# Performance work log

Measured on AMD Instinct MI355X. Metric: run time of the kernel, lower is better.

The kernel has to match this reference:

```python
import jax, jax.numpy as jnp
import numpy as np

N = 500_000
E = 8_000_000
DIM = 3
CG_ITERS = 20
CG_TOL = 1e-4


def setup_inputs() -> dict:
    key = jax.random.key(0)
    k0, k1, k2, k3, k4, k5 = jax.random.split(key, 6)
    u_hat = jax.random.normal(k0, (N, DIM), dtype=jnp.float32)
    edge_index = jax.random.randint(k1, (2, E), 0, N, dtype=jnp.int32)
    face_normals = jax.random.normal(k2, (E, DIM), dtype=jnp.float32)
    face_areas = jax.random.uniform(k3, (E,), dtype=jnp.float32)
    face_dists = jax.random.uniform(k4, (E,), dtype=jnp.float32)
    cell_volumes = jax.random.uniform(k5, (N,), dtype=jnp.float32)
    return {
        "u_hat": u_hat,
        "edge_index": edge_index,
        "face_normals": face_normals,
        "face_areas": face_areas,
        "face_dists": face_dists,
        "cell_volumes": cell_volumes,
    }


def _segsum(vals, idx, n):
    return jax.ops.segment_sum(vals, idx, num_segments=n)


def reference(u_hat, edge_index, face_normals, face_areas, face_dists, cell_volumes):
    src, dst = edge_index[0], edge_index[1]
    n = u_hat.shape[0]

    # --- compute_divergence: D_i = (1/V_i) sum flux over faces into i ---
    u_face = 0.5 * (u_hat[src] + u_hat[dst])                 # (E, dim)
    flux = jnp.sum(u_face * face_normals, axis=-1) * face_areas  # (E,)
    div = _segsum(flux, dst, n) / jnp.clip(cell_volumes, 1e-12)

    # --- build_laplacian_rhs ---
    w = face_areas / jnp.clip(face_dists, 1e-8)              # (E,)
    diag = _segsum(w, dst, n)                                # (N,)
    off = -w
    b = div

    # --- cg_solve with Jacobi preconditioner ---
    m_inv = 1.0 / jnp.clip(diag, 1e-8)

    def matvec(phi):
        return diag * phi + _segsum(off * phi[src], dst, n)

    phi0 = jnp.zeros_like(b)
    r0 = b - matvec(phi0)
    z0 = m_inv * r0
    p0 = z0
    rz0 = jnp.sum(r0 * z0)

    def step(state, _):
        phi, r, z, p, rz, done = state
        # torch checks ||r|| < tol and breaks before the update
        active = jnp.logical_and(~done, jnp.linalg.norm(r) >= CG_TOL)
        ap = matvec(p)
        alpha = rz / (jnp.sum(p * ap) + 1e-12)
        phi_n = phi + alpha * p
        r_n = r - alpha * ap
        z_n = m_inv * r_n
        rz_n = jnp.sum(r_n * z_n)
        beta = rz_n / (rz + 1e-12)
        p_n = z_n + beta * p
        sel = lambda a, b_: jnp.where(active, a, b_)
        new_state = (sel(phi_n, phi), sel(r_n, r), sel(z_n, z),
                     sel(p_n, p), jnp.where(active, rz_n, rz), ~active)
        return new_state, None

    (phi, _, _, _, _, _), _ = jax.lax.scan(
        step, (phi0, r0, z0, p0, rz0, jnp.array(False)), None, length=CG_ITERS)

    # --- apply_pressure_correction ---
    grad_term = (w * phi[src])[:, None] * face_normals       # (E, dim)
    grad_phi = _segsum(grad_term, dst, n) / jnp.clip(cell_volumes, 1e-12)[:, None]
    u_corrected = u_hat - grad_phi
    return u_corrected, phi
```

## Files before the change

kernel.cpp:

```cpp
#include <hip/hip_runtime.h>


#define TPB 256
#define KB 2048
#define CG_ITERS 20
#define TOL2 1e-8f

struct Sum3 { float a, b, c; };

__device__ inline Sum3 block_sum3_bcast(const float* __restrict__ A,
                                        const float* __restrict__ B,
                                        const float* __restrict__ C, int n) {
  float va = 0.f, vb = 0.f, vc = 0.f;
  for (int k = threadIdx.x; k < n; k += TPB) { va += A[k]; vb += B[k]; vc += C[k]; }
#pragma unroll
  for (int o = 32; o; o >>= 1) {
    va += __shfl_down(va, o, 64);
    vb += __shfl_down(vb, o, 64);
    vc += __shfl_down(vc, o, 64);
  }
  __shared__ float sa[TPB / 64], sb[TPB / 64], sc[TPB / 64], bc[3];
  int lane = threadIdx.x & 63, wid = threadIdx.x >> 6;
  if (lane == 0) { sa[wid] = va; sb[wid] = vb; sc[wid] = vc; }
  __syncthreads();
  if (threadIdx.x == 0) {
    float ta = 0.f, tb = 0.f, tc = 0.f;
#pragma unroll
    for (int k = 0; k < TPB / 64; k++) { ta += sa[k]; tb += sb[k]; tc += sc[k]; }
    bc[0] = ta; bc[1] = tb; bc[2] = tc;
  }
  __syncthreads();
  Sum3 r{bc[0], bc[1], bc[2]};
  __syncthreads();
  return r;
}

__device__ inline void block_reduce1_store(float v1, float* d1) {
#pragma unroll
  for (int o = 32; o; o >>= 1) v1 += __shfl_down(v1, o, 64);
  __shared__ float s1[TPB / 64];
  int lane = threadIdx.x & 63, wid = threadIdx.x >> 6;
  if (lane == 0) s1[wid] = v1;
  __syncthreads();
  if (threadIdx.x == 0) {
    float t1 = 0.f;
#pragma unroll
    for (int k = 0; k < TPB / 64; k++) t1 += s1[k];
    *d1 = t1;
  }
}

__device__ inline void block_reduce2_store(float v1, float v2, float* d1, float* d2) {
#pragma unroll
  for (int o = 32; o; o >>= 1) {
    v1 += __shfl_down(v1, o, 64);
    v2 += __shfl_down(v2, o, 64);
  }
  __shared__ float s1[TPB / 64], s2[TPB / 64];
  int lane = threadIdx.x & 63, wid = threadIdx.x >> 6;
  if (lane == 0) { s1[wid] = v1; s2[wid] = v2; }
  __syncthreads();
  if (threadIdx.x == 0) {
    float t1 = 0.f, t2 = 0.f;
#pragma unroll
    for (int k = 0; k < TPB / 64; k++) { t1 += s1[k]; t2 += s2[k]; }
    *d1 = t1;
    *d2 = t2;
  }
}

__global__ __launch_bounds__(TPB) void hist(
    const int* __restrict__ ei, unsigned* __restrict__ cnt,
    unsigned* __restrict__ rank, int E) {
  int e = blockIdx.x * TPB + threadIdx.x;
  if (e >= E) return;
  rank[e] = atomicAdd(&cnt[ei[E + e]], 1u);
}

__global__ __launch_bounds__(TPB) void scan_blocks(
    const unsigned* __restrict__ cnt, unsigned* __restrict__ offs,
    unsigned* __restrict__ btot, int n) {
  __shared__ unsigned sd[TPB];
  int t = threadIdx.x;
  int base = blockIdx.x * 1024 + t * 4;
  unsigned v0 = 0, v1 = 0, v2 = 0, v3 = 0;
  if (base + 0 < n) v0 = cnt[base + 0];
  if (base + 1 < n) v1 = cnt[base + 1];
  if (base + 2 < n) v2 = cnt[base + 2];
  if (base + 3 < n) v3 = cnt[base + 3];
  unsigned local = v0 + v1 + v2 + v3;
  sd[t] = local;
  __syncthreads();
  for (int o = 1; o < TPB; o <<= 1) {
    unsigned x = (t >= o) ? sd[t - o] : 0u;
    __syncthreads();
    sd[t] += x;
    __syncthreads();
  }
  unsigned excl = sd[t] - local;
  if (base + 0 < n) offs[base + 0] = excl; excl += v0;
  if (base + 1 < n) offs[base + 1] = excl; excl += v1;
  if (base + 2 < n) offs[base + 2] = excl; excl += v2;
  if (base + 3 < n) offs[base + 3] = excl;
  if (t == TPB - 1) btot[blockIdx.x] = sd[TPB - 1];
}

__global__ __launch_bounds__(512) void scan_totals(unsigned* __restrict__ btot, int nb) {
  __shared__ unsigned sd[512];
  int t = threadIdx.x;
  unsigned v = (t < nb) ? btot[t] : 0u;
  sd[t] = v;
  __syncthreads();
  for (int o = 1; o < 512; o <<= 1) {
    unsigned x = (t >= o) ? sd[t - o] : 0u;
    __syncthreads();
    sd[t] += x;
    __syncthreads();
  }
  if (t < nb) btot[t] = sd[t] - v;
}

__global__ __launch_bounds__(TPB) void scan_add(
    unsigned* __restrict__ offs, const unsigned* __restrict__ btot,
    int n, unsigned total) {
  int i = blockIdx.x * TPB + threadIdx.x;
  if (i < n) offs[i] += btot[i >> 10];
  if (i == 0) offs[n] = total;
}

__global__ __launch_bounds__(TPB) void scatter_edges(
    const int* __restrict__ ei, const float* __restrict__ u_hat,
    const float* __restrict__ fn, const float* __restrict__ fa,
    const float* __restrict__ fd, const unsigned* __restrict__ rank,
    const unsigned* __restrict__ offs, int2* __restrict__ csr_sw,
    int2* __restrict__ csr_ef, int E) {
  int e = blockIdx.x * TPB + threadIdx.x;
  if (e >= E) return;
  int s = ei[e], d = ei[E + e];
  float area = fa[e];
  float w = area / fmaxf(fd[e], 1e-8f);
  float ux = 0.5f * (u_hat[3 * s]     + u_hat[3 * d]);
  float uy = 0.5f * (u_hat[3 * s + 1] + u_hat[3 * d + 1]);
  float uz = 0.5f * (u_hat[3 * s + 2] + u_hat[3 * d + 2]);
  float flux = (ux * fn[3 * e] + uy * fn[3 * e + 1] + uz * fn[3 * e + 2]) * area;
  unsigned pos = offs[d] + rank[e];
  csr_sw[pos] = make_int2(s, __float_as_int(w));
  csr_ef[pos] = make_int2(e, __float_as_int(flux));
}

__global__ __launch_bounds__(TPB) void node_setup(
    const int2* __restrict__ csr_sw, const int2* __restrict__ csr_ef,
    const unsigned* __restrict__ offs, const float* __restrict__ cv,
    float* __restrict__ diag, float* __restrict__ r, float* __restrict__ p,
    float* __restrict__ phi, float* __restrict__ minv,
    float* __restrict__ rz_part, float* __restrict__ rr_part, int N) {
  const int gpb = TPB / 8;
  const int stride = KB * gpb;
  int g0 = blockIdx.x * gpb + (threadIdx.x >> 3);
  int l = threadIdx.x & 7;
  float rzacc = 0.f, rracc = 0.f;
  for (int g = g0; g < N; g += stride) {
    unsigned a = offs[g], bnd = offs[g + 1];
    float wsum = 0.f, fsum = 0.f;
    for (unsigned j = a + l; j < bnd; j += 8) {
      wsum += __int_as_float(csr_sw[j].y);
      fsum += __int_as_float(csr_ef[j].y);
    }
#pragma unroll
    for (int o = 4; o; o >>= 1) {
      wsum += __shfl_down(wsum, o, 8);
      fsum += __shfl_down(fsum, o, 8);
    }
    if (l == 0) {
      float vol = fmaxf(cv[g], 1e-12f);
      float b = fsum / vol;
      float mi = 1.0f / fmaxf(wsum, 1e-8f);
      diag[g] = wsum;
      minv[g] = mi;
      r[g] = b;
      phi[g] = 0.f;
      float pi = mi * b;
      p[g] = pi;
      rzacc += b * pi;
      rracc += b * b;
    }
  }
  block_reduce2_store(rzacc, rracc, &rz_part[blockIdx.x], &rr_part[blockIdx.x]);
}

__global__ __launch_bounds__(TPB) void matvec(
    const float* __restrict__ p, const float* __restrict__ diag,
    const unsigned* __restrict__ offs, const int2* __restrict__ csr_sw,
    float* __restrict__ ap, float* __restrict__ pap_part, int N) {
  const int gpb = TPB / 8;
  const int stride = KB * gpb;
  int g0 = blockIdx.x * gpb + (threadIdx.x >> 3);
  int l = threadIdx.x & 7;
  float acc = 0.f;
  for (int g = g0; g < N; g += stride) {
    unsigned a = offs[g], bnd = offs[g + 1];
    float sum = 0.f;
    for (unsigned j = a + l; j < bnd; j += 8) {
      int2 sw = csr_sw[j];
      sum += __int_as_float(sw.y) * p[sw.x];
    }
#pragma unroll
    for (int o = 4; o; o >>= 1) sum += __shfl_down(sum, o, 8);
    if (l == 0) {
      float pi = p[g];
      float api = diag[g] * pi - sum;
      ap[g] = api;
      acc += pi * api;
    }
  }
  block_reduce1_store(acc, &pap_part[blockIdx.x]);
}

__global__ __launch_bounds__(TPB) void cg_update(
    float* __restrict__ phi, float* __restrict__ r, const float* __restrict__ p,
    const float* __restrict__ ap, const float* __restrict__ minv,
    const float* __restrict__ pap_it, const float* __restrict__ rz_it,
    const float* __restrict__ rr_it, float* __restrict__ rz_next,
    float* __restrict__ rr_next, int N) {
  Sum3 s = block_sum3_bcast(pap_it, rz_it, rr_it, KB);
  bool act = (s.c >= TOL2);
  float alpha = s.b / (s.a + 1e-12f);
  float rzacc = 0.f, rracc = 0.f;
  for (int i = blockIdx.x * TPB + threadIdx.x; i < N; i += KB * TPB) {
    float ri = r[i];
    if (act) {
      phi[i] += alpha * p[i];
      ri -= alpha * ap[i];
      r[i] = ri;
    }
    float zi = minv[i] * ri;
    rzacc += ri * zi;
    rracc += ri * ri;
  }
  block_reduce2_store(rzacc, rracc, &rz_next[blockIdx.x], &rr_next[blockIdx.x]);
}

__global__ __launch_bounds__(TPB) void p_update(
    float* __restrict__ p, const float* __restrict__ r,
    const float* __restrict__ minv, const float* __restrict__ rz_next,
    const float* __restrict__ rz_it, const float* __restrict__ rr_it, int N) {
  Sum3 s = block_sum3_bcast(rz_next, rz_it, rr_it, KB);
  if (s.c < TOL2) return;
  float beta = s.a / (s.b + 1e-12f);
  for (int i = blockIdx.x * TPB + threadIdx.x; i < N; i += KB * TPB) {
    p[i] = minv[i] * r[i] + beta * p[i];
  }
}

__global__ __launch_bounds__(TPB) void finalize(
    const float* __restrict__ u_hat, const float* __restrict__ cv,
    const float* __restrict__ phi, const unsigned* __restrict__ offs,
    const int2* __restrict__ csr_sw, const int2* __restrict__ csr_ef,
    const float* __restrict__ fn, float* __restrict__ out, int N) {
  const int gpb = TPB / 8;
  const int stride = KB * gpb;
  int g0 = blockIdx.x * gpb + (threadIdx.x >> 3);
  int l = threadIdx.x & 7;
  for (int g = g0; g < N; g += stride) {
    unsigned a = offs[g], bnd = offs[g + 1];
    float gx = 0.f, gy = 0.f, gz = 0.f;
    for (unsigned j = a + l; j < bnd; j += 8) {
      int2 sw = csr_sw[j];
      float t = __int_as_float(sw.y) * phi[sw.x];
      int e = csr_ef[j].x;
      gx += t * fn[3 * e];
      gy += t * fn[3 * e + 1];
      gz += t * fn[3 * e + 2];
    }
#pragma unroll
    for (int o = 4; o; o >>= 1) {
      gx += __shfl_down(gx, o, 8);
      gy += __shfl_down(gy, o, 8);
      gz += __shfl_down(gz, o, 8);
    }
    if (l == 0) {
      float iv = 1.0f / fmaxf(cv[g], 1e-12f);
      out[3 * g]     = u_hat[3 * g]     - gx * iv;
      out[3 * g + 1] = u_hat[3 * g + 1] - gy * iv;
      out[3 * g + 2] = u_hat[3 * g + 2] - gz * iv;
      out[3 * N + g] = phi[g];
    }
  }
}

extern "C" void kernel_launch(void* const* d_in, const int* in_sizes, int n_in,
                              void* d_out, int out_size, void* d_ws, size_t ws_size,
                              hipStream_t stream) {
  const float* u_hat = (const float*)d_in[0];
  const int*   ei    = (const int*)d_in[1];
  const float* fn    = (const float*)d_in[2];
  const float* fa    = (const float*)d_in[3];
  const float* fd    = (const float*)d_in[4];
  const float* cv    = (const float*)d_in[5];
  float* out = (float*)d_out;

  const int N = in_sizes[0] / 3;
  const int E = in_sizes[1] / 2;

  char* base = (char*)d_ws;
  size_t off = 0;
  auto alloc = [&](size_t bytes) -> void* {
    void* ptr = base + off;
    off = (off + bytes + 255) & ~size_t(255);
    return ptr;
  };
  unsigned* cnt = (unsigned*)alloc((size_t)N * 4);
  size_t zero_bytes = off;
  unsigned* offs     = (unsigned*)alloc((size_t)(N + 1) * 4);
  unsigned* btot     = (unsigned*)alloc(512 * 4);
  unsigned* rank     = (unsigned*)alloc((size_t)E * 4);
  float*    diag     = (float*)alloc((size_t)N * 4);
  float*    minv     = (float*)alloc((size_t)N * 4);
  float*    phi      = (float*)alloc((size_t)N * 4);
  float*    rvec     = (float*)alloc((size_t)N * 4);
  float*    pvec     = (float*)alloc((size_t)N * 4);
  float*    ap       = (float*)alloc((size_t)N * 4);
  float*    rzrr     = (float*)alloc((size_t)(2 * (CG_ITERS + 1)) * KB * 4);
  float*    papp     = (float*)alloc((size_t)CG_ITERS * KB * 4);
  int2*     csr_sw   = (int2*)alloc((size_t)E * 8);
  int2*     csr_ef   = (int2*)alloc((size_t)E * 8);
  (void)ws_size; (void)n_in; (void)out_size;

  auto rz_part = [&](int it) { return rzrr + (size_t)(2 * it) * KB; };
  auto rr_part = [&](int it) { return rzrr + (size_t)(2 * it + 1) * KB; };
  auto pap_part = [&](int it) { return papp + (size_t)it * KB; };

  const int gridE = (E + TPB - 1) / TPB;
  const int gridN = (N + TPB - 1) / TPB;
  const int nbScan = (N + 1023) / 1024;

  hipMemsetAsync(base, 0, zero_bytes, stream);

  hist<<<gridE, TPB, 0, stream>>>(ei, cnt, rank, E);

  scan_blocks<<<nbScan, TPB, 0, stream>>>(cnt, offs, btot, N);
  scan_totals<<<1, 512, 0, stream>>>(btot, nbScan);
  scan_add<<<gridN, TPB, 0, stream>>>(offs, btot, N, (unsigned)E);

  scatter_edges<<<gridE, TPB, 0, stream>>>(ei, u_hat, fn, fa, fd, rank, offs,
                                           csr_sw, csr_ef, E);

  node_setup<<<KB, TPB, 0, stream>>>(csr_sw, csr_ef, offs, cv, diag,
                                     rvec, pvec, phi, minv,
                                     rz_part(0), rr_part(0), N);

  for (int it = 0; it < CG_ITERS; it++) {
    matvec<<<KB, TPB, 0, stream>>>(pvec, diag, offs, csr_sw, ap,
                                   pap_part(it), N);
    cg_update<<<KB, TPB, 0, stream>>>(phi, rvec, pvec, ap, minv,
                                      pap_part(it), rz_part(it), rr_part(it),
                                      rz_part(it + 1), rr_part(it + 1), N);
    if (it < CG_ITERS - 1) {
      p_update<<<KB, TPB, 0, stream>>>(pvec, rvec, minv,
                                       rz_part(it + 1), rz_part(it),
                                       rr_part(it), N);
    }
  }

  finalize<<<KB, TPB, 0, stream>>>(u_hat, cv, phi, offs, csr_sw, csr_ef,
                                   fn, out, N);
}
```

Before: 2.630 ms.

## Replace per-node CSR with 256-node bucketed edge layout and shared-memory accumulation

Edges are now grouped into buckets of 256 destination nodes with a two-pass, block-local counting sort. The old global-atomic histogram and per-edge rank array are gone. The source index and local destination are packed into one 64-bit word alongside the weight. The matvec, setup and finalize kernels process one bucket per block and accumulate into per-node shared-memory slots with LDS atomics, instead of 8-lane segmented reductions per node. This is meant to cut global atomic contention, remove divergence from variable row lengths, and shrink edge metadata traffic. The cost is LDS atomic contention and floating-point summation order that is no longer deterministic.

```diff
diff --git a/kernel.cpp b/kernel.cpp
--- a/kernel.cpp
+++ b/kernel.cpp
@@ -2,7 +2,10 @@
 
 
 #define TPB 256
+#define TPB_A 1024
 #define KB 2048
+#define NBLK 256
+#define MAXNB 2048
 #define CG_ITERS 20
 #define TOL2 1e-8f
 
@@ -69,12 +72,19 @@
   }
 }
 
-__global__ __launch_bounds__(TPB) void hist(
-    const int* __restrict__ ei, unsigned* __restrict__ cnt,
-    unsigned* __restrict__ rank, int E) {
-  int e = blockIdx.x * TPB + threadIdx.x;
-  if (e >= E) return;
-  rank[e] = atomicAdd(&cnt[ei[E + e]], 1u);
+__global__ __launch_bounds__(TPB_A) void bucket_hist(
+    const int* __restrict__ ei, unsigned* __restrict__ mat,
+    int E, int NB, int chunk) {
+  __shared__ unsigned cntL[MAXNB];
+  for (int i = threadIdx.x; i < NB; i += TPB_A) cntL[i] = 0;
+  __syncthreads();
+  int blk = blockIdx.x;
+  int e0 = blk * chunk, e1 = min(E, e0 + chunk);
+  for (int e = e0 + threadIdx.x; e < e1; e += TPB_A)
+    atomicAdd(&cntL[((unsigned)ei[E + e]) >> 8], 1u);
+  __syncthreads();
+  for (int b = threadIdx.x; b < NB; b += TPB_A)
+    mat[(size_t)b * NBLK + blk] = cntL[b];
 }
 
 __global__ __launch_bounds__(TPB) void scan_blocks(
@@ -128,92 +138,108 @@
   if (i == 0) offs[n] = total;
 }
 
-__global__ __launch_bounds__(TPB) void scatter_edges(
+__global__ __launch_bounds__(TPB_A) void bucket_place(
     const int* __restrict__ ei, const float* __restrict__ u_hat,
     const float* __restrict__ fn, const float* __restrict__ fa,
-    const float* __restrict__ fd, const unsigned* __restrict__ rank,
-    const unsigned* __restrict__ offs, int2* __restrict__ csr_sw,
-    int2* __restrict__ csr_ef, int E) {
-  int e = blockIdx.x * TPB + threadIdx.x;
-  if (e >= E) return;
-  int s = ei[e], d = ei[E + e];
-  float area = fa[e];
-  float w = area / fmaxf(fd[e], 1e-8f);
-  float ux = 0.5f * (u_hat[3 * s]     + u_hat[3 * d]);
-  float uy = 0.5f * (u_hat[3 * s + 1] + u_hat[3 * d + 1]);
-  float uz = 0.5f * (u_hat[3 * s + 2] + u_hat[3 * d + 2]);
-  float flux = (ux * fn[3 * e] + uy * fn[3 * e + 1] + uz * fn[3 * e + 2]) * area;
-  unsigned pos = offs[d] + rank[e];
-  csr_sw[pos] = make_int2(s, __float_as_int(w));
-  csr_ef[pos] = make_int2(e, __float_as_int(flux));
+    const float* __restrict__ fd, const unsigned* __restrict__ offs,
+    unsigned long long* __restrict__ A1, float* __restrict__ A2flux,
+    int* __restrict__ A3eid, int E, int NB, int chunk) {
+  __shared__ unsigned cntL[MAXNB];
+  __shared__ unsigned offL[MAXNB];
+  int blk = blockIdx.x;
+  for (int i = threadIdx.x; i < NB; i += TPB_A) {
+    cntL[i] = 0;
+    offL[i] = offs[(size_t)i * NBLK + blk];
+  }
+  __syncthreads();
+  int e0 = blk * chunk, e1 = min(E, e0 + chunk);
+  for (int e = e0 + threadIdx.x; e < e1; e += TPB_A) {
+    int s = ei[e], d = ei[E + e];
+    float area = fa[e];
+    float w = area / fmaxf(fd[e], 1e-8f);
+    float ux = 0.5f * (u_hat[3 * s]     + u_hat[3 * d]);
+    float uy = 0.5f * (u_hat[3 * s + 1] + u_hat[3 * d + 1]);
+    float uz = 0.5f * (u_hat[3 * s + 2] + u_hat[3 * d + 2]);
+    float flux = (ux * fn[3 * e] + uy * fn[3 * e + 1] + uz * fn[3 * e + 2]) * area;
+    unsigned b = ((unsigned)d) >> 8;
+    unsigned dl = ((unsigned)d) & 255u;
+    unsigned r = atomicAdd(&cntL[b], 1u);
+    unsigned pos = offL[b] + r;
+    unsigned hi = (dl << 19) | (unsigned)s;
+    A1[pos] = ((unsigned long long)hi << 32) | (unsigned long long)__float_as_uint(w);
+    A2flux[pos] = flux;
+    A3eid[pos] = e;
+  }
 }
 
 __global__ __launch_bounds__(TPB) void node_setup(
-    const int2* __restrict__ csr_sw, const int2* __restrict__ csr_ef,
+    const unsigned long long* __restrict__ A1, const float* __restrict__ A2flux,
     const unsigned* __restrict__ offs, const float* __restrict__ cv,
     float* __restrict__ diag, float* __restrict__ r, float* __restrict__ p,
     float* __restrict__ phi, float* __restrict__ minv,
-    float* __restrict__ rz_part, float* __restrict__ rr_part, int N) {
-  const int gpb = TPB / 8;
-  const int stride = KB * gpb;
-  int g0 = blockIdx.x * gpb + (threadIdx.x >> 3);
-  int l = threadIdx.x & 7;
-  float rzacc = 0.f, rracc = 0.f;
-  for (int g = g0; g < N; g += stride) {
-    unsigned a = offs[g], bnd = offs[g + 1];
-    float wsum = 0.f, fsum = 0.f;
-    for (unsigned j = a + l; j < bnd; j += 8) {
-      wsum += __int_as_float(csr_sw[j].y);
-      fsum += __int_as_float(csr_ef[j].y);
-    }
-#pragma unroll
-    for (int o = 4; o; o >>= 1) {
-      wsum += __shfl_down(wsum, o, 8);
-      fsum += __shfl_down(fsum, o, 8);
-    }
-    if (l == 0) {
-      float vol = fmaxf(cv[g], 1e-12f);
-      float b = fsum / vol;
+    float* __restrict__ rz_part, float* __restrict__ rr_part, int N, int NB) {
+  __shared__ float wacc[256], facc[256];
+  int b = blockIdx.x;
+  float rzv = 0.f, rrv = 0.f;
+  if (b < NB) {
+    wacc[threadIdx.x] = 0.f;
+    facc[threadIdx.x] = 0.f;
+    __syncthreads();
+    unsigned jb = offs[(size_t)b * NBLK], je = offs[(size_t)(b + 1) * NBLK];
+    for (unsigned j = jb + threadIdx.x; j < je; j += TPB) {
+      unsigned long long v = A1[j];
+      unsigned hi = (unsigned)(v >> 32);
+      float w = __uint_as_float((unsigned)v);
+      atomicAdd(&wacc[hi >> 19], w);
+      atomicAdd(&facc[hi >> 19], A2flux[j]);
+    }
+    __syncthreads();
+    int node = (b << 8) + threadIdx.x;
+    if (node < N) {
+      float wsum = wacc[threadIdx.x];
+      float vol = fmaxf(cv[node], 1e-12f);
+      float bval = facc[threadIdx.x] / vol;
       float mi = 1.0f / fmaxf(wsum, 1e-8f);
-      diag[g] = wsum;
-      minv[g] = mi;
-      r[g] = b;
-      phi[g] = 0.f;
-      float pi = mi * b;
-      p[g] = pi;
-      rzacc += b * pi;
-      rracc += b * b;
-    }
-  }
-  block_reduce2_store(rzacc, rracc, &rz_part[blockIdx.x], &rr_part[blockIdx.x]);
+      diag[node] = wsum;
+      minv[node] = mi;
+      r[node] = bval;
+      phi[node] = 0.f;
+      float pi = mi * bval;
+      p[node] = pi;
+      rzv = bval * pi;
+      rrv = bval * bval;
+    }
+  }
+  block_reduce2_store(rzv, rrv, &rz_part[blockIdx.x], &rr_part[blockIdx.x]);
 }
 
 __global__ __launch_bounds__(TPB) void matvec(
     const float* __restrict__ p, const float* __restrict__ diag,
-    const unsigned* __restrict__ offs, const int2* __restrict__ csr_sw,
-    float* __restrict__ ap, float* __restrict__ pap_part, int N) {
-  const int gpb = TPB / 8;
-  const int stride = KB * gpb;
-  int g0 = blockIdx.x * gpb + (threadIdx.x >> 3);
-  int l = threadIdx.x & 7;
-  float acc = 0.f;
-  for (int g = g0; g < N; g += stride) {
-    unsigned a = offs[g], bnd = offs[g + 1];
-    float sum = 0.f;
-    for (unsigned j = a + l; j < bnd; j += 8) {
-      int2 sw = csr_sw[j];
-      sum += __int_as_float(sw.y) * p[sw.x];
-    }
-#pragma unroll
-    for (int o = 4; o; o >>= 1) sum += __shfl_down(sum, o, 8);
-    if (l == 0) {
-      float pi = p[g];
-      float api = diag[g] * pi - sum;
-      ap[g] = api;
-      acc += pi * api;
-    }
-  }
-  block_reduce1_store(acc, &pap_part[blockIdx.x]);
+    const unsigned* __restrict__ offs, const unsigned long long* __restrict__ A1,
+    float* __restrict__ ap, float* __restrict__ pap_part, int N, int NB) {
+  __shared__ float acc[256];
+  int b = blockIdx.x;
+  float contrib = 0.f;
+  if (b < NB) {
+    acc[threadIdx.x] = 0.f;
+    __syncthreads();
+    unsigned jb = offs[(size_t)b * NBLK], je = offs[(size_t)(b + 1) * NBLK];
+    for (unsigned j = jb + threadIdx.x; j < je; j += TPB) {
+      unsigned long long v = A1[j];
+      unsigned hi = (unsigned)(v >> 32);
+      float w = __uint_as_float((unsigned)v);
+      atomicAdd(&acc[hi >> 19], w * p[hi & 0x7FFFFu]);
+    }
+    __syncthreads();
+    int node = (b << 8) + threadIdx.x;
+    if (node < N) {
+      float pi = p[node];
+      float api = diag[node] * pi - acc[threadIdx.x];
+      ap[node] = api;
+      contrib = pi * api;
+    }
+  }
+  block_reduce1_store(contrib, &pap_part[blockIdx.x]);
 }
 
 __global__ __launch_bounds__(TPB) void cg_update(
@@ -255,36 +281,35 @@
 __global__ __launch_bounds__(TPB) void finalize(
     const float* __restrict__ u_hat, const float* __restrict__ cv,
     const float* __restrict__ phi, const unsigned* __restrict__ offs,
-    const int2* __restrict__ csr_sw, const int2* __restrict__ csr_ef,
-    const float* __restrict__ fn, float* __restrict__ out, int N) {
-  const int gpb = TPB / 8;
-  const int stride = KB * gpb;
-  int g0 = blockIdx.x * gpb + (threadIdx.x >> 3);
-  int l = threadIdx.x & 7;
-  for (int g = g0; g < N; g += stride) {
-    unsigned a = offs[g], bnd = offs[g + 1];
-    float gx = 0.f, gy = 0.f, gz = 0.f;
-    for (unsigned j = a + l; j < bnd; j += 8) {
-      int2 sw = csr_sw[j];
-      float t = __int_as_float(sw.y) * phi[sw.x];
-      int e = csr_ef[j].x;
-      gx += t * fn[3 * e];
-      gy += t * fn[3 * e + 1];
-      gz += t * fn[3 * e + 2];
-    }
-#pragma unroll
-    for (int o = 4; o; o >>= 1) {
-      gx += __shfl_down(gx, o, 8);
-      gy += __shfl_down(gy, o, 8);
-      gz += __shfl_down(gz, o, 8);
-    }
-    if (l == 0) {
-      float iv = 1.0f / fmaxf(cv[g], 1e-12f);
-      out[3 * g]     = u_hat[3 * g]     - gx * iv;
-      out[3 * g + 1] = u_hat[3 * g + 1] - gy * iv;
-      out[3 * g + 2] = u_hat[3 * g + 2] - gz * iv;
-      out[3 * N + g] = phi[g];
-    }
+    const unsigned long long* __restrict__ A1, const int* __restrict__ A3eid,
+    const float* __restrict__ fn, float* __restrict__ out, int N, int NB) {
+  __shared__ float gxa[256], gya[256], gza[256];
+  int b = blockIdx.x;
+  if (b >= NB) return;
+  gxa[threadIdx.x] = 0.f;
+  gya[threadIdx.x] = 0.f;
+  gza[threadIdx.x] = 0.f;
+  __syncthreads();
+  unsigned jb = offs[(size_t)b * NBLK], je = offs[(size_t)(b + 1) * NBLK];
+  for (unsigned j = jb + threadIdx.x; j < je; j += TPB) {
+    unsigned long long v = A1[j];
+    unsigned hi = (unsigned)(v >> 32);
+    float w = __uint_as_float((unsigned)v);
+    float t = w * phi[hi & 0x7FFFFu];
+    int e = A3eid[j];
+    int dl = hi >> 19;
+    atomicAdd(&gxa[dl], t * fn[3 * e]);
+    atomicAdd(&gya[dl], t * fn[3 * e + 1]);
+    atomicAdd(&gza[dl], t * fn[3 * e + 2]);
+  }
+  __syncthreads();
+  int node = (b << 8) + threadIdx.x;
+  if (node < N) {
+    float iv = 1.0f / fmaxf(cv[node], 1e-12f);
+    out[3 * node]     = u_hat[3 * node]     - gxa[threadIdx.x] * iv;
+    out[3 * node + 1] = u_hat[3 * node + 1] - gya[threadIdx.x] * iv;
+    out[3 * node + 2] = u_hat[3 * node + 2] - gza[threadIdx.x] * iv;
+    out[3 * N + node] = phi[node];
   }
 }
 
@@ -301,6 +326,9 @@
 
   const int N = in_sizes[0] / 3;
   const int E = in_sizes[1] / 2;
+  const int NB = (N + 255) >> 8;
+  const int NS = NB * NBLK;
+  const int chunk = (E + NBLK - 1) / NBLK;
 
   char* base = (char*)d_ws;
   size_t off = 0;
@@ -309,49 +337,45 @@
     off = (off + bytes + 255) & ~size_t(255);
     return ptr;
   };
-  unsigned* cnt = (unsigned*)alloc((size_t)N * 4);
-  size_t zero_bytes = off;
-  unsigned* offs     = (unsigned*)alloc((size_t)(N + 1) * 4);
-  unsigned* btot     = (unsigned*)alloc(512 * 4);
-  unsigned* rank     = (unsigned*)alloc((size_t)E * 4);
-  float*    diag     = (float*)alloc((size_t)N * 4);
-  float*    minv     = (float*)alloc((size_t)N * 4);
-  float*    phi      = (float*)alloc((size_t)N * 4);
-  float*    rvec     = (float*)alloc((size_t)N * 4);
-  float*    pvec     = (float*)alloc((size_t)N * 4);
-  float*    ap       = (float*)alloc((size_t)N * 4);
-  float*    rzrr     = (float*)alloc((size_t)(2 * (CG_ITERS + 1)) * KB * 4);
-  float*    papp     = (float*)alloc((size_t)CG_ITERS * KB * 4);
-  int2*     csr_sw   = (int2*)alloc((size_t)E * 8);
-  int2*     csr_ef   = (int2*)alloc((size_t)E * 8);
+  unsigned* mat   = (unsigned*)alloc((size_t)NS * 4);
+  unsigned* offs  = (unsigned*)alloc((size_t)(NS + 1) * 4);
+  unsigned* btot  = (unsigned*)alloc(512 * 4);
+  float*    diag  = (float*)alloc((size_t)N * 4);
+  float*    minv  = (float*)alloc((size_t)N * 4);
+  float*    phi   = (float*)alloc((size_t)N * 4);
+  float*    rvec  = (float*)alloc((size_t)N * 4);
+  float*    pvec  = (float*)alloc((size_t)N * 4);
+  float*    ap    = (float*)alloc((size_t)N * 4);
+  float*    rzrr  = (float*)alloc((size_t)(2 * (CG_ITERS + 1)) * KB * 4);
+  float*    papp  = (float*)alloc((size_t)CG_ITERS * KB * 4);
+  unsigned long long* A1 = (unsigned long long*)alloc((size_t)E * 8);
+  float*    A2flux = (float*)alloc((size_t)E * 4);
+  int*      A3eid  = (int*)alloc((size_t)E * 4);
   (void)ws_size; (void)n_in; (void)out_size;
 
   auto rz_part = [&](int it) { return rzrr + (size_t)(2 * it) * KB; };
   auto rr_part = [&](int it) { return rzrr + (size_t)(2 * it + 1) * KB; };
   auto pap_part = [&](int it) { return papp + (size_t)it * KB; };
 
-  const int gridE = (E + TPB - 1) / TPB;
-  const int gridN = (N + TPB - 1) / TPB;
-  const int nbScan = (N + 1023) / 1024;
-
-  hipMemsetAsync(base, 0, zero_bytes, stream);
-
-  hist<<<gridE, TPB, 0, stream>>>(ei, cnt, rank, E);
-
-  scan_blocks<<<nbScan, TPB, 0, stream>>>(cnt, offs, btot, N);
+  const int nbScan = (NS + 1023) / 1024;
+  const int gridScanAdd = (NS + TPB - 1) / TPB;
+
+  bucket_hist<<<NBLK, TPB_A, 0, stream>>>(ei, mat, E, NB, chunk);
+
+  scan_blocks<<<nbScan, TPB, 0, stream>>>(mat, offs, btot, NS);
   scan_totals<<<1, 512, 0, stream>>>(btot, nbScan);
-  scan_add<<<gridN, TPB, 0, stream>>>(offs, btot, N, (unsigned)E);
-
-  scatter_edges<<<gridE, TPB, 0, stream>>>(ei, u_hat, fn, fa, fd, rank, offs,
-                                           csr_sw, csr_ef, E);
-
-  node_setup<<<KB, TPB, 0, stream>>>(csr_sw, csr_ef, offs, cv, diag,
+  scan_add<<<gridScanAdd, TPB, 0, stream>>>(offs, btot, NS, (unsigned)E);
+
+  bucket_place<<<NBLK, TPB_A, 0, stream>>>(ei, u_hat, fn, fa, fd, offs,
+                                           A1, A2flux, A3eid, E, NB, chunk);
+
+  node_setup<<<KB, TPB, 0, stream>>>(A1, A2flux, offs, cv, diag,
                                      rvec, pvec, phi, minv,
-                                     rz_part(0), rr_part(0), N);
+                                     rz_part(0), rr_part(0), N, NB);
 
   for (int it = 0; it < CG_ITERS; it++) {
-    matvec<<<KB, TPB, 0, stream>>>(pvec, diag, offs, csr_sw, ap,
-                                   pap_part(it), N);
+    matvec<<<KB, TPB, 0, stream>>>(pvec, diag, offs, A1, ap,
+                                   pap_part(it), N, NB);
     cg_update<<<KB, TPB, 0, stream>>>(phi, rvec, pvec, ap, minv,
                                       pap_part(it), rz_part(it), rr_part(it),
                                       rz_part(it + 1), rr_part(it + 1), N);
@@ -362,6 +386,6 @@
     }
   }
 
-  finalize<<<KB, TPB, 0, stream>>>(u_hat, cv, phi, offs, csr_sw, csr_ef,
-                                   fn, out, N);
-}
+  finalize<<<NB, TPB, 0, stream>>>(u_hat, cv, phi, offs, A1, A3eid,
+                                   fn, out, N, NB);
+}
```

Measured after the change: 2.516 ms. 1.05x faster.
